# Optimization experiments

Measured on AMD Instinct MI355X. Metric: run time of the kernel, lower is better.

Reference implementation:

```python
import jax, jax.numpy as jnp
import numpy as np

# Model dims (match init_kwargs / input_specs)
B, L, D = 4, 1024, 512
CHI, S = 32, 4          # bond_dim, spatial_bond_dim
TRUNC_THR = 1e-4        # relative SVD truncation threshold
LN_EPS = 1e-6


def setup_inputs() -> dict:
    key = jax.random.key(0)
    ks = jax.random.split(key, 6)
    def dense(k, fi, fo):
        return jax.random.normal(k, (fi, fo), jnp.float32) / np.float32(np.sqrt(fi))
    return {
        "x": jax.random.normal(ks[0], (B, L, D), jnp.float32),
        "W_site": dense(ks[1], D, CHI * S * CHI),
        "b_site": jnp.zeros((CHI * S * CHI,), jnp.float32),
        "W_bridge": dense(ks[2], S * CHI, CHI),
        "b_bridge": jnp.zeros((CHI,), jnp.float32),
        "W_out": dense(ks[3], CHI, D),
        "b_out": jnp.zeros((D,), jnp.float32),
        "gamma": jnp.ones((D,), jnp.float32),
        "beta": jnp.zeros((D,), jnp.float32),
        "W_gate": dense(ks[4], D, D),
        "b_gate": jnp.zeros((D,), jnp.float32),
    }


def _mps_temporal_scan(x, site_weights):
    """Sequential O(L*chi^2) MPS scan with per-step SVD truncation.

    x: [B, L, D]; site_weights: [B, L, chi, s, chi].
    State h_t [B, chi] is the (normalized) left environment vector. Each step
    contracts the left vector (state + input injection from the first chi
    features, since initial_state is zeros) with the site tensor, truncates
    small singular values (relative threshold), and accumulates log-norms.
    Returns outputs [B, L, s*chi] and log_probs [B, L].
    """
    u_seq = jnp.transpose(x[:, :, :CHI], (1, 0, 2))            # [L, B, chi]
    A_seq = jnp.transpose(site_weights, (1, 0, 2, 3, 4))        # [L, B, chi, s, chi]

    def step(h, inp):
        A, u = inp                                              # [B,chi,s,chi], [B,chi]
        left = h + u                                            # input-driven left vector
        M = jnp.einsum('bl,blpr->bpr', left, A)                 # [B, s, chi]
        U, Sv, Vh = jnp.linalg.svd(M, full_matrices=False)      # Sv: [B, min(s,chi)]
        mask = (Sv >= TRUNC_THR * Sv[:, :1]).astype(M.dtype)    # relative truncation
        St = Sv * mask
        Mt = jnp.einsum('bik,bk,bkr->bir', U, St, Vh)           # truncated site matrix
        nrm = jnp.sqrt(jnp.sum(St * St, axis=-1) + 1e-12)       # Frobenius norm -> log prob
        v = jnp.sum(Mt, axis=1)                                 # contract physical index
        h_new = v / (jnp.linalg.norm(v, axis=-1, keepdims=True) + 1e-12)
        return h_new, (Mt.reshape(Mt.shape[0], -1), jnp.log(nrm))

    h0 = jnp.zeros((x.shape[0], CHI), x.dtype)                  # initial_state = zeros
    _, (outs, logp) = jax.lax.scan(step, h0, (A_seq, u_seq))
    return jnp.transpose(outs, (1, 0, 2)), jnp.transpose(logp, (1, 0))


def reference(x, W_site, b_site, W_bridge, b_bridge, W_out, b_out,
              gamma, beta, W_gate, b_gate):
    x = x.astype(jnp.float32)
    Bb, Ll = x.shape[0], x.shape[1]
    # site_tensor_proj: Dense(chi*s*chi) applied directly to inputs
    site_weights = (x @ W_site + b_site).reshape(Bb, Ll, CHI, S, CHI)
    outs, _logp = _mps_temporal_scan(x, site_weights)           # [B, L, s*chi]
    y = outs @ W_bridge + b_bridge                              # mps_bridge -> [B,L,chi]
    y = y @ W_out + b_out                                       # output_projection -> [B,L,D]
    # LayerNorm(eps=1e-6)
    mu = jnp.mean(y, axis=-1, keepdims=True)
    var = jnp.mean((y - mu) ** 2, axis=-1, keepdims=True)
    yn = (y - mu) * jax.lax.rsqrt(var + LN_EPS) * gamma + beta
    # gated residual
    gate = jax.nn.sigmoid(x @ W_gate + b_gate)
    return gate * yn + (1.0 - gate) * x
```

## Files before the change

### kernel.cpp

```cpp
#include <hip/hip_runtime.h>
#include <math.h>

#define B_   4
#define L_   1024
#define D_   512
#define CHI_ 32
#define S_   4
#define BT_  (B_ * L_)
#define NC_  2560
#define DPRE 8

__device__ __forceinline__ float readlane_f(float v, int l) {
    return __int_as_float(__builtin_amdgcn_readlane(__float_as_int(v), l));
}

__device__ __forceinline__ float bpermute_f(int byte_idx, float v) {
    return __int_as_float(__builtin_amdgcn_ds_bpermute(byte_idx, __float_as_int(v)));
}

template <int CTRL>
__device__ __forceinline__ float dpp_add(float x) {
    int y = __builtin_amdgcn_update_dpp(0, __float_as_int(x), CTRL, 0xf, 0xf, true);
    return x + __int_as_float(y);
}

__device__ __forceinline__ float reduce32_to_lane31(float x) {
    x = dpp_add<0x111>(x);
    x = dpp_add<0x112>(x);
    x = dpp_add<0x114>(x);
    x = dpp_add<0x118>(x);
    x = dpp_add<0x142>(x);
    return x;
}

__device__ __forceinline__ float octet_sum(float x) {
    x = dpp_add<0x111>(x);
    x = dpp_add<0x112>(x);
    x = dpp_add<0x114>(x);
    return x;
}

__global__ __launch_bounds__(256) void buildW_kernel(
    const float* __restrict__ Ws, const float* __restrict__ bs,
    const float* __restrict__ Wb, const float* __restrict__ Wg,
    const float* __restrict__ bg, float* __restrict__ Wcomb,
    float* __restrict__ biasC)
{
    const int tid = threadIdx.x;

    if (blockIdx.x == 512) {
        for (int f = tid; f < NC_; f += 256) {
            float acc;
            if (f < 1024) {
                const int q = f >> 8, rem = f & 255, i = rem >> 2, e = rem & 3;
                const int l = 4 * (i & 7) + e, r = (i >> 3) + 8 * q;
                const float* p = bs + l * 128 + r;
                acc = p[0] + p[32] + p[64] + p[96];
            } else if (f < 2048) {
                const int g = f - 1024, l = g >> 5, j = g & 31;
                acc = 0.f;
                for (int pr = 0; pr < 128; ++pr)
                    acc = fmaf(bs[l * 128 + pr], Wb[pr * 32 + j], acc);
            } else {
                acc = bg[f - 2048];
            }
            biasC[f] = acc;
        }
        return;
    }

    __shared__ float wsrow[4096];
    __shared__ float wbs[4096];

    const int d = blockIdx.x;
    #pragma unroll
    for (int i = 0; i < 16; ++i) {
        wsrow[i * 256 + tid] = Ws[(size_t)d * 4096 + i * 256 + tid];
        wbs[i * 256 + tid]   = Wb[i * 256 + tid];
    }
    __syncthreads();

    float* wrow = Wcomb + (size_t)d * NC_;

    #pragma unroll
    for (int ii = 0; ii < 4; ++ii) {
        const int f = ii * 256 + tid;
        const int q = f >> 8, rem = f & 255, i = rem >> 2, e = rem & 3;
        const int l = 4 * (i & 7) + e, r = (i >> 3) + 8 * q;
        const float* p = wsrow + l * 128 + r;
        wrow[f] = p[0] + p[32] + p[64] + p[96];
    }
    #pragma unroll
    for (int ii = 0; ii < 4; ++ii) {
        const int g = ii * 256 + tid;
        const int l = g >> 5, j = g & 31;
        float acc = 0.f;
        #pragma unroll 8
        for (int pr = 0; pr < 128; ++pr)
            acc = fmaf(wsrow[l * 128 + pr], wbs[pr * 32 + j], acc);
        wrow[1024 + g] = acc;
    }
    #pragma unroll
    for (int ii = 0; ii < 2; ++ii) {
        const int c = ii * 256 + tid;
        wrow[2048 + c] = Wg[(size_t)d * 512 + c];
    }
}

__global__ __launch_bounds__(256) void gemm_bias_kernel(
    const float* __restrict__ A, const float* __restrict__ Bm,
    const float* __restrict__ bias, float* __restrict__ C,
    int M, int N, int K)
{
    __shared__ float As[32][68];
    __shared__ float Bs[32][64];

    const int tid = threadIdx.x;
    const int tx = tid & 15;
    const int ty = tid >> 4;
    const int m0 = blockIdx.y * 64;
    const int n0 = blockIdx.x * 64;

    float c[4][4] = {};

    for (int k0 = 0; k0 < K; k0 += 32) {
        {
            const int o = tid * 8;
            const int m = o >> 5;
            const int k = o & 31;
            const float* ap = A + (size_t)(m0 + m) * K + k0 + k;
            const float4 a0 = *(const float4*)ap;
            const float4 a1 = *(const float4*)(ap + 4);
            As[k + 0][m] = a0.x; As[k + 1][m] = a0.y;
            As[k + 2][m] = a0.z; As[k + 3][m] = a0.w;
            As[k + 4][m] = a1.x; As[k + 5][m] = a1.y;
            As[k + 6][m] = a1.z; As[k + 7][m] = a1.w;
        }
        {
            const int o = tid * 8;
            const int k = o >> 6;
            const int n = o & 63;
            const float* bp = Bm + (size_t)(k0 + k) * N + n0 + n;
            *(float4*)&Bs[k][n]     = *(const float4*)bp;
            *(float4*)&Bs[k][n + 4] = *(const float4*)(bp + 4);
        }
        __syncthreads();

        #pragma unroll
        for (int kk = 0; kk < 32; ++kk) {
            const float4 av = *(const float4*)&As[kk][ty * 4];
            const float4 bv = *(const float4*)&Bs[kk][tx * 4];
            const float a[4] = {av.x, av.y, av.z, av.w};
            const float b[4] = {bv.x, bv.y, bv.z, bv.w};
            #pragma unroll
            for (int i = 0; i < 4; ++i)
                #pragma unroll
                for (int j = 0; j < 4; ++j)
                    c[i][j] = fmaf(a[i], b[j], c[i][j]);
        }
        __syncthreads();
    }

    const float4 bv = *(const float4*)&bias[n0 + tx * 4];
    #pragma unroll
    for (int i = 0; i < 4; ++i) {
        float4 outv;
        outv.x = c[i][0] + bv.x;
        outv.y = c[i][1] + bv.y;
        outv.z = c[i][2] + bv.z;
        outv.w = c[i][3] + bv.w;
        *(float4*)&C[(size_t)(m0 + ty * 4 + i) * N + n0 + tx * 4] = outv;
    }
}

__device__ __forceinline__ void gemm_tile_body(
    const float* __restrict__ A, const float* __restrict__ Bm,
    const float* __restrict__ bias, float* __restrict__ C,
    int M, int N, int K, int m0, int n0,
    float (*As)[132], float (*Bs)[132])
{
    const int tid = threadIdx.x;
    const int tx = tid & 15;
    const int ty = tid >> 4;

    float acc[8][8] = {};

    for (int k0 = 0; k0 < K; k0 += 32) {
        #pragma unroll
        for (int p = 0; p < 4; ++p) {
            const int m = (tid >> 3) + 32 * p;
            const int k = (tid & 7) * 4;
            const float4 av = *(const float4*)(A + (size_t)(m0 + m) * K + k0 + k);
            As[k + 0][m] = av.x;
            As[k + 1][m] = av.y;
            As[k + 2][m] = av.z;
            As[k + 3][m] = av.w;
        }
        #pragma unroll
        for (int p = 0; p < 2; ++p) {
            const int k = (tid >> 4) + 16 * p;
            const int n = (tid & 15) * 8;
            const float* bp = Bm + (size_t)(k0 + k) * N + n0 + n;
            *(float4*)&Bs[k][n]     = *(const float4*)bp;
            *(float4*)&Bs[k][n + 4] = *(const float4*)(bp + 4);
        }
        __syncthreads();

        #pragma unroll
        for (int kk = 0; kk < 32; ++kk) {
            const float4 a0 = *(const float4*)&As[kk][ty * 8];
            const float4 a1 = *(const float4*)&As[kk][ty * 8 + 4];
            const float4 b0 = *(const float4*)&Bs[kk][tx * 8];
            const float4 b1 = *(const float4*)&Bs[kk][tx * 8 + 4];
            const float a[8] = {a0.x, a0.y, a0.z, a0.w, a1.x, a1.y, a1.z, a1.w};
            const float b[8] = {b0.x, b0.y, b0.z, b0.w, b1.x, b1.y, b1.z, b1.w};
            #pragma unroll
            for (int i = 0; i < 8; ++i)
                #pragma unroll
                for (int j = 0; j < 8; ++j)
                    acc[i][j] = fmaf(a[i], b[j], acc[i][j]);
        }
        __syncthreads();
    }

    const float4 bv0 = *(const float4*)&bias[n0 + tx * 8];
    const float4 bv1 = *(const float4*)&bias[n0 + tx * 8 + 4];
    #pragma unroll
    for (int i = 0; i < 8; ++i) {
        float* cp = C + (size_t)(m0 + ty * 8 + i) * N + n0 + tx * 8;
        float4 o0, o1;
        o0.x = acc[i][0] + bv0.x; o0.y = acc[i][1] + bv0.y;
        o0.z = acc[i][2] + bv0.z; o0.w = acc[i][3] + bv0.w;
        o1.x = acc[i][4] + bv1.x; o1.y = acc[i][5] + bv1.y;
        o1.z = acc[i][6] + bv1.z; o1.w = acc[i][7] + bv1.w;
        *(float4*)cp       = o0;
        *(float4*)(cp + 4) = o1;
    }
}

__global__ __launch_bounds__(256) void cvec_kernel(
    const float* __restrict__ Cc, const float* __restrict__ x,
    float* __restrict__ cBuf)
{
    const int tid  = threadIdx.x;
    const int lane = tid & 63;
    const int bt   = blockIdx.x * 4 + (tid >> 6);

    const float* base = Cc + (size_t)bt * NC_ + 4 * lane;
    float4 a0 = *(const float4*)(base + 0);
    float4 a1 = *(const float4*)(base + 256);
    float4 a2 = *(const float4*)(base + 512);
    float4 a3 = *(const float4*)(base + 768);

    const float u = x[(size_t)bt * D_ + (lane & 31)];
    const int idx0 = 16 * (lane & 7);
    const float u0 = bpermute_f(idx0 + 0,  u);
    const float u1 = bpermute_f(idx0 + 4,  u);
    const float u2 = bpermute_f(idx0 + 8,  u);
    const float u3 = bpermute_f(idx0 + 12, u);

    float p0 = fmaf(u3, a0.w, fmaf(u2, a0.z, fmaf(u1, a0.y, u0 * a0.x)));
    float p1 = fmaf(u3, a1.w, fmaf(u2, a1.z, fmaf(u1, a1.y, u0 * a1.x)));
    float p2 = fmaf(u3, a2.w, fmaf(u2, a2.z, fmaf(u1, a2.y, u0 * a2.x)));
    float p3 = fmaf(u3, a3.w, fmaf(u2, a3.z, fmaf(u1, a3.y, u0 * a3.x)));

    p0 = octet_sum(p0); p1 = octet_sum(p1);
    p2 = octet_sum(p2); p3 = octet_sum(p3);

    if ((lane & 7) == 7) {
        const int k = lane >> 3;
        float* cp = cBuf + (size_t)bt * 32 + k;
        cp[0]  = p0;
        cp[8]  = p1;
        cp[16] = p2;
        cp[24] = p3;
    }
}

__global__ __launch_bounds__(256) void fused_scan_gemm2_kernel(
    const float* __restrict__ x, const float* __restrict__ Wcomb,
    const float* __restrict__ biasC, float* __restrict__ Cc,
    const float* __restrict__ cBuf, float* __restrict__ wOut)
{
    __shared__ float As[32][132];
    __shared__ float Bs[32][132];

    if (blockIdx.x < 4) {
        const int tid = threadIdx.x;
        if (tid >= 64) return;
        const int b = blockIdx.x;

        const float* At = Cc + (size_t)b * L_ * NC_ + 4 * tid;
        const float* cb = cBuf + (size_t)b * L_ * 32 + (tid & 31);
        float*       wo = wOut + (size_t)b * L_ * 64 + tid;

        const int idx0 = 16 * (tid & 7);
        const int idxR = 32 * (tid & 7) + 28;
        const bool selA = (tid >> 3) & 1;
        const bool selB = (tid >> 4) & 1;

        float4 areg[DPRE][4];
        float  creg[DPRE];

        #pragma unroll
        for (int j = 0; j < DPRE; ++j) {
            const float* ap = At + (size_t)j * NC_;
            #pragma unroll
            for (int q = 0; q < 4; ++q) areg[j][q] = *(const float4*)(ap + 256 * q);
            creg[j] = cb[j * 32];
        }

        float w = 0.f;

        for (int t = 0; t < L_; t += DPRE) {
            #pragma unroll
            for (int j = 0; j < DPRE; ++j) {
                wo[(t + j) * 64] = w;

                float red = reduce32_to_lane31(w * w);

                const float wb0 = bpermute_f(idx0 + 0,  w);
                const float wb1 = bpermute_f(idx0 + 4,  w);
                const float wb2 = bpermute_f(idx0 + 8,  w);
                const float wb3 = bpermute_f(idx0 + 12, w);

                float p0, p1, p2, p3;
                {
                    const float4 a0 = areg[j][0], a1 = areg[j][1];
                    const float4 a2 = areg[j][2], a3 = areg[j][3];
                    p0 = fmaf(wb3, a0.w, fmaf(wb2, a0.z, fmaf(wb1, a0.y, wb0 * a0.x)));
                    p1 = fmaf(wb3, a1.w, fmaf(wb2, a1.z, fmaf(wb1, a1.y, wb0 * a1.x)));
                    p2 = fmaf(wb3, a2.w, fmaf(wb2, a2.z, fmaf(wb1, a2.y, wb0 * a2.x)));
                    p3 = fmaf(wb3, a3.w, fmaf(wb2, a3.z, fmaf(wb1, a3.y, wb0 * a3.x)));
                }

                p0 = octet_sum(p0);
                p1 = octet_sum(p1);
                p2 = octet_sum(p2);
                p3 = octet_sum(p3);

                const float m0 = bpermute_f(idxR, p0);
                const float m1 = bpermute_f(idxR, p1);
                const float m2 = bpermute_f(idxR, p2);
                const float m3 = bpermute_f(idxR, p3);
                const float t0 = selA ? m1 : m0;
                const float t1 = selA ? m3 : m2;
                const float m  = selB ? t1 : t0;

                const float n2 = readlane_f(red, 31);
                const float rn = rsqrtf(n2 + 1e-24f);
                w = fmaf(m, rn, creg[j]);

                int tn = t + j + DPRE;
                if (tn > L_ - 1) tn = L_ - 1;
                const float* ap = At + (size_t)tn * NC_;
                #pragma unroll
                for (int q = 0; q < 4; ++q) areg[j][q] = *(const float4*)(ap + 256 * q);
                creg[j] = cb[tn * 32];
            }
        }
        return;
    }

    const int g  = blockIdx.x - 4;
    const int m0 = (g / 12) * 128;
    const int n0 = 1024 + (g % 12) * 128;
    gemm_tile_body(x, Wcomb, biasC, Cc, BT_, NC_, D_, m0, n0, As, Bs);
}

__global__ __launch_bounds__(128) void phaseB_kernel(
    const float* __restrict__ Cc, const float* __restrict__ x,
    const float* __restrict__ wBuf, const float* __restrict__ bb,
    float* __restrict__ y1)
{
    __shared__ float lf[32];
    __shared__ float part[4][32];

    const int bt = blockIdx.x;
    const int tid = threadIdx.x;

    if (tid < 64) {
        const float wv = wBuf[(size_t)bt * 64 + tid];
        float red = reduce32_to_lane31(wv * wv);
        const float n2 = readlane_f(red, 31);
        const float rn = rsqrtf(n2 + 1e-24f);
        if (tid < 32)
            lf[tid] = fmaf(wv, rn, x[(size_t)bt * D_ + tid]);
    }
    __syncthreads();

    const int j = tid & 31, q = tid >> 5;
    const float* Gp = Cc + (size_t)bt * NC_ + 1024;
    float p = 0.f;
    #pragma unroll
    for (int i = 0; i < 8; ++i)
        p = fmaf(lf[8 * q + i], Gp[(8 * q + i) * 32 + j], p);
    part[q][j] = p;
    __syncthreads();

    if (tid < 32)
        y1[bt * 32 + tid] = part[0][tid] + part[1][tid] + part[2][tid]
                          + part[3][tid] + bb[tid];
}

__global__ __launch_bounds__(256) void epilogue_kernel(
    const float* __restrict__ x, const float* __restrict__ y1buf,
    const float* __restrict__ Wout, const float* __restrict__ bout,
    const float* __restrict__ gamma, const float* __restrict__ beta,
    const float* __restrict__ Cc, float* __restrict__ out)
{
    __shared__ float ys[32];
    __shared__ float red1[4], red2[4];

    const int bt = blockIdx.x;
    const int tid = threadIdx.x;

    if (tid < 32) ys[tid] = y1buf[bt * 32 + tid];
    __syncthreads();

    float yv[2];
    #pragma unroll
    for (int q = 0; q < 2; ++q) {
        const int d = tid + q * 256;
        float acc = bout[d];
        #pragma unroll
        for (int j = 0; j < 32; ++j)
            acc = fmaf(ys[j], Wout[j * D_ + d], acc);
        yv[q] = acc;
    }

    float s1 = yv[0] + yv[1];
    float s2 = yv[0] * yv[0] + yv[1] * yv[1];
    #pragma unroll
    for (int m = 1; m <= 32; m <<= 1) {
        s1 += __shfl_xor(s1, m);
        s2 += __shfl_xor(s2, m);
    }
    const int wid = tid >> 6;
    if ((tid & 63) == 0) { red1[wid] = s1; red2[wid] = s2; }
    __syncthreads();
    const float S1 = red1[0] + red1[1] + red1[2] + red1[3];
    const float S2 = red2[0] + red2[1] + red2[2] + red2[3];
    const float mu  = S1 * (1.f / (float)D_);
    const float var = S2 * (1.f / (float)D_) - mu * mu;
    const float rstd = rsqrtf(var + 1e-6f);

    #pragma unroll
    for (int q = 0; q < 2; ++q) {
        const int d = tid + q * 256;
        const size_t gi = (size_t)bt * D_ + d;
        const float yn = (yv[q] - mu) * rstd * gamma[d] + beta[d];
        const float z = Cc[(size_t)bt * NC_ + 2048 + d];
        const float g = 1.f / (1.f + expf(-z));
        const float xv = x[gi];
        out[gi] = g * yn + (1.f - g) * xv;
    }
}

extern "C" void kernel_launch(void* const* d_in, const int* in_sizes, int n_in,
                              void* d_out, int out_size, void* d_ws, size_t ws_size,
                              hipStream_t stream)
{
    const float* x        = (const float*)d_in[0];
    const float* W_site   = (const float*)d_in[1];
    const float* b_site   = (const float*)d_in[2];
    const float* W_bridge = (const float*)d_in[3];
    const float* b_bridge = (const float*)d_in[4];
    const float* W_out    = (const float*)d_in[5];
    const float* b_out    = (const float*)d_in[6];
    const float* gamma    = (const float*)d_in[7];
    const float* beta     = (const float*)d_in[8];
    const float* W_gate   = (const float*)d_in[9];
    const float* b_gate   = (const float*)d_in[10];
    float* out = (float*)d_out;

    float* ws = (float*)d_ws;
    float* Wcomb = ws;
    float* biasC = Wcomb + (size_t)512 * NC_;
    float* Cc    = biasC + NC_;
    float* cBuf  = Cc    + (size_t)BT_ * NC_;
    float* wBuf  = cBuf  + (size_t)BT_ * 32;
    float* y1    = wBuf  + (size_t)BT_ * 64;

    buildW_kernel<<<dim3(513), dim3(256), 0, stream>>>(
        W_site, b_site, W_bridge, W_gate, b_gate, Wcomb, biasC);

    gemm_bias_kernel<<<dim3(16, 64), dim3(256), 0, stream>>>(
        x, Wcomb, biasC, Cc, BT_, NC_, D_);

    cvec_kernel<<<dim3(BT_ / 4), dim3(256), 0, stream>>>(Cc, x, cBuf);

    fused_scan_gemm2_kernel<<<dim3(4 + 12 * (BT_ / 128)), dim3(256), 0, stream>>>(
        x, Wcomb, biasC, Cc, cBuf, wBuf);

    phaseB_kernel<<<dim3(BT_), dim3(128), 0, stream>>>(
        Cc, x, wBuf, b_bridge, y1);

    epilogue_kernel<<<dim3(BT_), dim3(256), 0, stream>>>(
        x, y1, W_out, b_out, gamma, beta, Cc, out);
}
```

Before: 389.5 us.

## Split weight build to overlap with first GEMM; fuse phaseB into epilogue

Weight preparation is split in two. A light kernel now writes only the column-sum block and the biases. The bridge-product and gate-copy columns are built by extra blocks of the first GEMM's launch. That GEMM only reads the first 1024 columns, so the two pieces can run concurrently. Separately, the phaseB reduction is merged into the epilogue kernel (now 256 threads), which removes a launch and the y1 round trip through global memory. The risk is a larger combined GEMM grid and different block scheduling.

```diff
diff --git a/kernel.cpp b/kernel.cpp
--- a/kernel.cpp
+++ b/kernel.cpp
@@ -40,11 +40,10 @@
     return x;
 }
 
-__global__ __launch_bounds__(256) void buildW_kernel(
+__global__ __launch_bounds__(256) void buildWA_kernel(
     const float* __restrict__ Ws, const float* __restrict__ bs,
-    const float* __restrict__ Wb, const float* __restrict__ Wg,
-    const float* __restrict__ bg, float* __restrict__ Wcomb,
-    float* __restrict__ biasC)
+    const float* __restrict__ Wb, const float* __restrict__ bg,
+    float* __restrict__ Wcomb, float* __restrict__ biasC)
 {
     const int tid = threadIdx.x;
 
@@ -70,14 +69,11 @@
     }
 
     __shared__ float wsrow[4096];
-    __shared__ float wbs[4096];
 
     const int d = blockIdx.x;
     #pragma unroll
-    for (int i = 0; i < 16; ++i) {
+    for (int i = 0; i < 16; ++i)
         wsrow[i * 256 + tid] = Ws[(size_t)d * 4096 + i * 256 + tid];
-        wbs[i * 256 + tid]   = Wb[i * 256 + tid];
-    }
     __syncthreads();
 
     float* wrow = Wcomb + (size_t)d * NC_;
@@ -90,36 +86,58 @@
         const float* p = wsrow + l * 128 + r;
         wrow[f] = p[0] + p[32] + p[64] + p[96];
     }
-    #pragma unroll
-    for (int ii = 0; ii < 4; ++ii) {
-        const int g = ii * 256 + tid;
-        const int l = g >> 5, j = g & 31;
-        float acc = 0.f;
-        #pragma unroll 8
-        for (int pr = 0; pr < 128; ++pr)
-            acc = fmaf(wsrow[l * 128 + pr], wbs[pr * 32 + j], acc);
-        wrow[1024 + g] = acc;
-    }
-    #pragma unroll
-    for (int ii = 0; ii < 2; ++ii) {
-        const int c = ii * 256 + tid;
-        wrow[2048 + c] = Wg[(size_t)d * 512 + c];
-    }
-}
-
-__global__ __launch_bounds__(256) void gemm_bias_kernel(
-    const float* __restrict__ A, const float* __restrict__ Bm,
-    const float* __restrict__ bias, float* __restrict__ C,
-    int M, int N, int K)
-{
-    __shared__ float As[32][68];
-    __shared__ float Bs[32][64];
+}
+
+__global__ __launch_bounds__(256) void gemm1_buildWB_kernel(
+    const float* __restrict__ x, const float* __restrict__ Ws,
+    const float* __restrict__ Wb, const float* __restrict__ Wg,
+    float* Wcomb, const float* __restrict__ biasC, float* __restrict__ C)
+{
+    __shared__ __align__(16) float smem[8192];
 
     const int tid = threadIdx.x;
+
+    if (blockIdx.x < 512) {
+        float* wsrow = smem;
+        float* wbs   = smem + 4096;
+
+        const int d = blockIdx.x;
+        #pragma unroll
+        for (int i = 0; i < 16; ++i) {
+            wsrow[i * 256 + tid] = Ws[(size_t)d * 4096 + i * 256 + tid];
+            wbs[i * 256 + tid]   = Wb[i * 256 + tid];
+        }
+        __syncthreads();
+
+        float* wrow = Wcomb + (size_t)d * NC_;
+
+        #pragma unroll
+        for (int ii = 0; ii < 4; ++ii) {
+            const int g = ii * 256 + tid;
+            const int l = g >> 5, j = g & 31;
+            float acc = 0.f;
+            #pragma unroll 8
+            for (int pr = 0; pr < 128; ++pr)
+                acc = fmaf(wsrow[l * 128 + pr], wbs[pr * 32 + j], acc);
+            wrow[1024 + g] = acc;
+        }
+        #pragma unroll
+        for (int ii = 0; ii < 2; ++ii) {
+            const int c = ii * 256 + tid;
+            wrow[2048 + c] = Wg[(size_t)d * 512 + c];
+        }
+        return;
+    }
+
+    float (*As)[68] = (float(*)[68])smem;
+    float (*Bs)[64] = (float(*)[64])(smem + 32 * 68);
+
+    const int g  = blockIdx.x - 512;
+    const int m0 = (g >> 4) * 64;
+    const int n0 = (g & 15) * 64;
     const int tx = tid & 15;
     const int ty = tid >> 4;
-    const int m0 = blockIdx.y * 64;
-    const int n0 = blockIdx.x * 64;
+    const int K = D_, N = NC_;
 
     float c[4][4] = {};
 
@@ -128,7 +146,7 @@
             const int o = tid * 8;
             const int m = o >> 5;
             const int k = o & 31;
-            const float* ap = A + (size_t)(m0 + m) * K + k0 + k;
+            const float* ap = x + (size_t)(m0 + m) * K + k0 + k;
             const float4 a0 = *(const float4*)ap;
             const float4 a1 = *(const float4*)(ap + 4);
             As[k + 0][m] = a0.x; As[k + 1][m] = a0.y;
@@ -140,7 +158,7 @@
             const int o = tid * 8;
             const int k = o >> 6;
             const int n = o & 63;
-            const float* bp = Bm + (size_t)(k0 + k) * N + n0 + n;
+            const float* bp = Wcomb + (size_t)(k0 + k) * N + n0 + n;
             *(float4*)&Bs[k][n]     = *(const float4*)bp;
             *(float4*)&Bs[k][n + 4] = *(const float4*)(bp + 4);
         }
@@ -161,7 +179,7 @@
         __syncthreads();
     }
 
-    const float4 bv = *(const float4*)&bias[n0 + tx * 4];
+    const float4 bv = *(const float4*)&biasC[n0 + tx * 4];
     #pragma unroll
     for (int i = 0; i < 4; ++i) {
         float4 outv;
@@ -368,13 +386,17 @@
     gemm_tile_body(x, Wcomb, biasC, Cc, BT_, NC_, D_, m0, n0, As, Bs);
 }
 
-__global__ __launch_bounds__(128) void phaseB_kernel(
+__global__ __launch_bounds__(256) void phaseB_epilogue_kernel(
     const float* __restrict__ Cc, const float* __restrict__ x,
     const float* __restrict__ wBuf, const float* __restrict__ bb,
-    float* __restrict__ y1)
+    const float* __restrict__ Wout, const float* __restrict__ bout,
+    const float* __restrict__ gamma, const float* __restrict__ beta,
+    float* __restrict__ out)
 {
     __shared__ float lf[32];
-    __shared__ float part[4][32];
+    __shared__ float part[8][32];
+    __shared__ float ys[32];
+    __shared__ float red1[4], red2[4];
 
     const int bt = blockIdx.x;
     const int tid = threadIdx.x;
@@ -389,33 +411,23 @@
     }
     __syncthreads();
 
-    const int j = tid & 31, q = tid >> 5;
-    const float* Gp = Cc + (size_t)bt * NC_ + 1024;
-    float p = 0.f;
-    #pragma unroll
-    for (int i = 0; i < 8; ++i)
-        p = fmaf(lf[8 * q + i], Gp[(8 * q + i) * 32 + j], p);
-    part[q][j] = p;
+    {
+        const int j = tid & 31, q = tid >> 5;
+        const float* Gp = Cc + (size_t)bt * NC_ + 1024;
+        float p = 0.f;
+        #pragma unroll
+        for (int i = 0; i < 4; ++i)
+            p = fmaf(lf[4 * q + i], Gp[(4 * q + i) * 32 + j], p);
+        part[q][j] = p;
+    }
     __syncthreads();
 
-    if (tid < 32)
-        y1[bt * 32 + tid] = part[0][tid] + part[1][tid] + part[2][tid]
-                          + part[3][tid] + bb[tid];
-}
-
-__global__ __launch_bounds__(256) void epilogue_kernel(
-    const float* __restrict__ x, const float* __restrict__ y1buf,
-    const float* __restrict__ Wout, const float* __restrict__ bout,
-    const float* __restrict__ gamma, const float* __restrict__ beta,
-    const float* __restrict__ Cc, float* __restrict__ out)
-{
-    __shared__ float ys[32];
-    __shared__ float red1[4], red2[4];
-
-    const int bt = blockIdx.x;
-    const int tid = threadIdx.x;
-
-    if (tid < 32) ys[tid] = y1buf[bt * 32 + tid];
+    if (tid < 32) {
+        float s = bb[tid];
+        #pragma unroll
+        for (int q = 0; q < 8; ++q) s += part[q][tid];
+        ys[tid] = s;
+    }
     __syncthreads();
 
     float yv[2];
@@ -480,22 +492,18 @@
     float* Cc    = biasC + NC_;
     float* cBuf  = Cc    + (size_t)BT_ * NC_;
     float* wBuf  = cBuf  + (size_t)BT_ * 32;
-    float* y1    = wBuf  + (size_t)BT_ * 64;
-
-    buildW_kernel<<<dim3(513), dim3(256), 0, stream>>>(
-        W_site, b_site, W_bridge, W_gate, b_gate, Wcomb, biasC);
-
-    gemm_bias_kernel<<<dim3(16, 64), dim3(256), 0, stream>>>(
-        x, Wcomb, biasC, Cc, BT_, NC_, D_);
+
+    buildWA_kernel<<<dim3(513), dim3(256), 0, stream>>>(
+        W_site, b_site, W_bridge, b_gate, Wcomb, biasC);
+
+    gemm1_buildWB_kernel<<<dim3(512 + 1024), dim3(256), 0, stream>>>(
+        x, W_site, W_bridge, W_gate, Wcomb, biasC, Cc);
 
     cvec_kernel<<<dim3(BT_ / 4), dim3(256), 0, stream>>>(Cc, x, cBuf);
 
     fused_scan_gemm2_kernel<<<dim3(4 + 12 * (BT_ / 128)), dim3(256), 0, stream>>>(
         x, Wcomb, biasC, Cc, cBuf, wBuf);
 
-    phaseB_kernel<<<dim3(BT_), dim3(128), 0, stream>>>(
-        Cc, x, wBuf, b_bridge, y1);
-
-    epilogue_kernel<<<dim3(BT_), dim3(256), 0, stream>>>(
-        x, y1, W_out, b_out, gamma, beta, Cc, out);
-}
+    phaseB_epilogue_kernel<<<dim3(BT_), dim3(256), 0, stream>>>(
+        Cc, x, wBuf, b_bridge, W_out, b_out, gamma, beta, out);
+}
```

Result: no change. 386.4 us (-0.8%).
